# Kernel tuning notes

Hardware: AMD Instinct MI355X
Metric: run time of the kernel (lower is better)

The kernel has to match this reference:

```python
import jax, jax.numpy as jnp
import numpy as np

L = 4


def make_coord(h, w):
    # pixel-center coords in [-1,1], shape (h*w, 2), dim order (y, x)
    ys = -1.0 + 1.0 / h + (2.0 / h) * jnp.arange(h, dtype=jnp.float32)
    xs = -1.0 + 1.0 / w + (2.0 / w) * jnp.arange(w, dtype=jnp.float32)
    gy, gx = jnp.meshgrid(ys, xs, indexing='ij')
    return jnp.stack([gy, gx], axis=-1).reshape(-1, 2)


def bilinear_sample(feat, gx, gy):
    # feat: (B,C,H,W); gx,gy in [-1,1], shape (B,N); align_corners=True
    B, C, H, W = feat.shape
    ix = (gx + 1.0) * 0.5 * (W - 1)
    iy = (gy + 1.0) * 0.5 * (H - 1)
    x0f = jnp.floor(ix)
    y0f = jnp.floor(iy)
    x0 = jnp.clip(x0f.astype(jnp.int32), 0, W - 1)
    x1 = jnp.clip(x0 + 1, 0, W - 1)
    y0 = jnp.clip(y0f.astype(jnp.int32), 0, H - 1)
    y1 = jnp.clip(y0 + 1, 0, H - 1)
    wx1 = ix - x0f
    wx0 = 1.0 - wx1
    wy1 = iy - y0f
    wy0 = 1.0 - wy1
    featf = feat.reshape(B, C, H * W)

    def g(yi, xi):
        idx = yi * W + xi  # (B,N)
        return jnp.take_along_axis(featf, idx[:, None, :], axis=2)  # (B,C,N)

    out = (g(y0, x0) * (wy0 * wx0)[:, None, :] + g(y0, x1) * (wy0 * wx1)[:, None, :]
           + g(y1, x0) * (wy1 * wx0)[:, None, :] + g(y1, x1) * (wy1 * wx1)[:, None, :])
    return out.transpose(0, 2, 1)  # (B,N,C)


def pos_enc(x):
    # x: (B,N,2) -> (B,N,4L); per dim: [sin_0..sin_{L-1}, cos_0..cos_{L-1}]
    freq = (2.0 ** jnp.arange(L, dtype=jnp.float32)) * np.pi
    spec = x[..., None] * freq  # (B,N,2,L)
    enc = jnp.concatenate([jnp.sin(spec), jnp.cos(spec)], axis=-1)  # (B,N,2,2L)
    return enc.reshape(*x.shape[:-1], 4 * L)


def mlp(x, w0, b0, w1, b1, w2, b2, w3, b3):
    h = jax.nn.relu(x @ w0 + b0)
    h = jax.nn.relu(h @ w1 + b1)
    h = jax.nn.relu(h @ w2 + b2)
    return h @ w3 + b3


def setup_inputs() -> dict:
    key = jax.random.key(0)
    ks = jax.random.split(key, 8)
    B, C, H, W = 4, 64, 128, 128
    hid, out_dim = 256, 3
    in_dim = C + 2 + 4 * L + 2  # 84
    s = 0.05
    return {
        'inp': jax.random.normal(ks[0], (B, C, H, W), jnp.float32),
        'w0': jax.random.normal(ks[1], (in_dim, hid), jnp.float32) * s,
        'b0': jnp.zeros((hid,), jnp.float32),
        'w1': jax.random.normal(ks[2], (hid, hid), jnp.float32) * s,
        'b1': jnp.zeros((hid,), jnp.float32),
        'w2': jax.random.normal(ks[3], (hid, hid), jnp.float32) * s,
        'b2': jnp.zeros((hid,), jnp.float32),
        'w3': jax.random.normal(ks[4], (hid, out_dim), jnp.float32) * s,
        'b3': jnp.zeros((out_dim,), jnp.float32),
        'scale': 2,
    }


def reference(inp, w0, b0, w1, b1, w2, b2, w3, b3, scale):
    B, C, H, W = inp.shape
    th, tw = int(round(H * scale)), int(round(W * scale))
    N = th * tw
    coord = jnp.broadcast_to(make_coord(th, tw)[None], (B, N, 2))
    # cell = (2/th, 2/tw); rel_cell = cell * (H, W)
    rel_cell = jnp.broadcast_to(
        jnp.array([2.0 / th * H, 2.0 / tw * W], jnp.float32), (B, N, 2))
    # feature-pixel coordinate map, appended as extra channels so one gather serves both
    fc = make_coord(H, W).reshape(H, W, 2).transpose(2, 0, 1)  # (2,H,W)
    aug = jnp.concatenate([inp, jnp.broadcast_to(fc[None], (B, 2, H, W))], axis=1)

    pe = pos_enc(coord)  # same for all 4 ensemble branches
    hw_scale = jnp.array([H, W], jnp.float32)
    rx, ry = 1.0 / H, 1.0 / W
    eps = 1e-6

    preds, areas = [], []
    for vx in (-1, 1):
        for vy in (-1, 1):
            c0 = jnp.clip(coord[..., 0] + vx * rx + eps, -1 + 1e-6, 1 - 1e-6)
            c1 = jnp.clip(coord[..., 1] + vy * ry + eps, -1 + 1e-6, 1 - 1e-6)
            # grid_sample uses (x, y) = flipped coord -> gx=c1, gy=c0
            q = bilinear_sample(aug, c1, c0)  # (B,N,C+2)
            q_feat, q_coord = q[..., :C], q[..., C:]
            rel = (coord - q_coord) * hw_scale  # (B,N,2)
            x = jnp.concatenate([q_feat, rel, pe, rel_cell], axis=-1)
            preds.append(mlp(x, w0, b0, w1, b1, w2, b2, w3, b3))
            areas.append(jnp.abs(rel[..., 0] * rel[..., 1]) + 1e-9)

    areas = [areas[3], areas[2], areas[1], areas[0]]  # diagonal swap
    tot = areas[0] + areas[1] + areas[2] + areas[3]
    ret = sum(p * (a / tot)[..., None] for p, a in zip(preds, areas))  # (B,N,out)
    return ret.reshape(B, th, tw, -1).transpose(0, 3, 1, 2)  # (B,out,th,tw)
```

## Files before the change

### kernel.cpp

```cpp
#include <hip/hip_runtime.h>
#include <math.h>

#define NB 4
#define NH 128
#define NW 128
#define TH 256
#define TW 256
#define AST 264
#define K0 96
#define MROWS 256
#define PIXB 64

typedef _Float16 f16;
typedef f16  f16x8 __attribute__((ext_vector_type(8)));
typedef f16  f16x4v __attribute__((ext_vector_type(4)));
typedef float f32x4 __attribute__((ext_vector_type(4)));
typedef float f32x16 __attribute__((ext_vector_type(16)));

#define OFF_W1 24576
#define OFF_W2 (OFF_W1 + 65536)
#define OFF_W3 (OFF_W2 + 65536)
#define OFF_PE (OFF_W3 + 4096)
#define WS_W_ELEMS (OFF_PE + 4096)
#define FT_ELEMS (NB * NH * NW * 64)

__device__ __forceinline__ void gload_lds16(const f16* g, f16* l) {
  __builtin_amdgcn_global_load_lds(
      (const __attribute__((address_space(1))) void*)(g),
      (__attribute__((address_space(3))) void*)(l), 16, 0, 0);
}

__global__ void cvt_weights(const float* __restrict__ w0, const float* __restrict__ w1,
                            const float* __restrict__ w2, const float* __restrict__ w3,
                            f16* __restrict__ ws) {
  const int i = blockIdx.x * 256 + threadIdx.x;
  if (i < 24576) {
    const int n = i / 96, k = i - n * 96;
    ws[i] = (k < 84) ? (f16)w0[k * 256 + n] : (f16)0.f;
  } else if (i < OFF_W2) {
    const int j = i - OFF_W1; const int n = j >> 8, k = j & 255;
    ws[i] = (f16)w1[k * 256 + n];
  } else if (i < OFF_W3) {
    const int j = i - OFF_W2; const int n = j >> 8, k = j & 255;
    ws[i] = (f16)w2[k * 256 + n];
  } else if (i < OFF_PE) {
    const int j = i - OFF_W3; const int n = j >> 8, k = j & 255;
    ws[i] = (n < 3) ? (f16)w3[k * 3 + n] : (f16)0.f;
  } else if (i < WS_W_ELEMS) {
    const int j = i - OFF_PE;
    const int o = (j & 2047) >> 3, e = j & 7;
    const float c = (2.0f * o + 1.0f) / 256.0f - 1.0f;
    const float f = (float)(1 << (e & 3)) * (float)M_PI;
    ws[i] = (f16)((e < 4) ? sinf(c * f) : cosf(c * f));
  }
}

__global__ void transpose_feat(const float* __restrict__ feat, f16* __restrict__ ft) {
  __shared__ f16 tile[64][66];
  const int bid = blockIdx.x;
  const int xt = bid & 1, y = (bid >> 1) & 127, b = bid >> 8;
  const int x0 = xt * 64;
  {
    const int c4 = threadIdx.x >> 6, x = threadIdx.x & 63;
#pragma unroll
    for (int co = 0; co < 16; ++co) {
      const int c = co * 4 + c4;
      tile[x][c] = (f16)feat[((size_t)(b * 64 + c) * NH + y) * NW + x0 + x];
    }
  }
  __syncthreads();
  {
    const int x4 = threadIdx.x >> 6, c = threadIdx.x & 63;
#pragma unroll
    for (int xo = 0; xo < 16; ++xo) {
      const int x = xo * 4 + x4;
      ft[((size_t)(b * NH + y) * NW + x0 + x) * 64 + c] = tile[x][c];
    }
  }
}

template<int K>
__device__ __forceinline__ void dense_layer(const f16* __restrict__ Wt,
                                            const float* __restrict__ bias,
                                            f16* act, f16* wlds,
                                            int wm, int wn, int l, int tid) {
  constexpr int NK = K / 16;
  const int lo = l & 31, hi = l >> 5;
  const int sn = tid & 255, sh = tid >> 8;
  const f16* src = Wt + (size_t)sn * K + sh * 8;
  f16* wdst = wlds + (tid >> 6) * 512;
  const f16* Bbase = act + (wm * 128 + lo) * AST + hi * 8;

  f32x16 acc[2][4];
#pragma unroll
  for (int nt = 0; nt < 2; ++nt) {
    f32x16 ci;
#pragma unroll
    for (int g = 0; g < 4; ++g) {
      const float4 b4 = *(const float4*)(bias + wn * 64 + nt * 32 + 8 * g + 4 * hi);
      ci[4 * g + 0] = b4.x; ci[4 * g + 1] = b4.y; ci[4 * g + 2] = b4.z; ci[4 * g + 3] = b4.w;
    }
#pragma unroll
    for (int mt = 0; mt < 4; ++mt) acc[nt][mt] = ci;
  }

  gload_lds16(src + 0 * 16, wdst + 0 * 4096);
  gload_lds16(src + 1 * 16, wdst + 1 * 4096);
  asm volatile("s_waitcnt vmcnt(1)" ::: "memory");
  __builtin_amdgcn_s_barrier();

#pragma unroll
  for (int ks = 0; ks < NK; ++ks) {
    if (ks + 2 < NK)
      gload_lds16(src + (ks + 2) * 16, wdst + ((ks + 2) % 3) * 4096);

    const f16* wb = wlds + (ks % 3) * 4096 + hi * 2048;
    const f16x8 A0 = *(const f16x8*)(wb + (wn * 64 + 0 * 32 + lo) * 8);
    const f16x8 A1 = *(const f16x8*)(wb + (wn * 64 + 1 * 32 + lo) * 8);
    const f16x8 B0 = *(const f16x8*)(Bbase + 0 * 32 * AST + ks * 16);
    const f16x8 B1 = *(const f16x8*)(Bbase + 1 * 32 * AST + ks * 16);
    const f16x8 B2 = *(const f16x8*)(Bbase + 2 * 32 * AST + ks * 16);
    const f16x8 B3 = *(const f16x8*)(Bbase + 3 * 32 * AST + ks * 16);

    __builtin_amdgcn_s_setprio(1);
    acc[0][0] = __builtin_amdgcn_mfma_f32_32x32x16_f16(A0, B0, acc[0][0], 0, 0, 0);
    acc[0][1] = __builtin_amdgcn_mfma_f32_32x32x16_f16(A0, B1, acc[0][1], 0, 0, 0);
    acc[0][2] = __builtin_amdgcn_mfma_f32_32x32x16_f16(A0, B2, acc[0][2], 0, 0, 0);
    acc[0][3] = __builtin_amdgcn_mfma_f32_32x32x16_f16(A0, B3, acc[0][3], 0, 0, 0);
    acc[1][0] = __builtin_amdgcn_mfma_f32_32x32x16_f16(A1, B0, acc[1][0], 0, 0, 0);
    acc[1][1] = __builtin_amdgcn_mfma_f32_32x32x16_f16(A1, B1, acc[1][1], 0, 0, 0);
    acc[1][2] = __builtin_amdgcn_mfma_f32_32x32x16_f16(A1, B2, acc[1][2], 0, 0, 0);
    acc[1][3] = __builtin_amdgcn_mfma_f32_32x32x16_f16(A1, B3, acc[1][3], 0, 0, 0);
    __builtin_amdgcn_s_setprio(0);

    asm volatile("s_waitcnt vmcnt(1)" ::: "memory");
    __builtin_amdgcn_s_barrier();
  }

#pragma unroll
  for (int nt = 0; nt < 2; ++nt)
#pragma unroll
    for (int mt = 0; mt < 4; ++mt)
#pragma unroll
      for (int g = 0; g < 4; ++g) {
        f16x4v o;
        o[0] = (f16)fmaxf(acc[nt][mt][4 * g + 0], 0.f);
        o[1] = (f16)fmaxf(acc[nt][mt][4 * g + 1], 0.f);
        o[2] = (f16)fmaxf(acc[nt][mt][4 * g + 2], 0.f);
        o[3] = (f16)fmaxf(acc[nt][mt][4 * g + 3], 0.f);
        *(f16x4v*)(act + (size_t)(wm * 128 + mt * 32 + lo) * AST +
                   wn * 64 + nt * 32 + 8 * g + 4 * hi) = o;
      }
}

template<bool USE_FT>
__global__ __launch_bounds__(512, 2) void inr2d_mfma(
    const float* __restrict__ feat, const f16* __restrict__ ft,
    const float* __restrict__ b0, const float* __restrict__ b1,
    const float* __restrict__ b2, const float* __restrict__ b3,
    const f16* __restrict__ ws, float* __restrict__ out)
{
  __shared__ f16 act[MROWS][AST];
  __shared__ f16 wlds[3 * 4096];
  __shared__ float area_s[MROWS];
  __shared__ f16 pred_s[MROWS][4];

  const int t = threadIdx.x;
  const int blk = ((blockIdx.x & 7) << 9) | (blockIdx.x >> 3);

  {
    const int r = t >> 1, sub = t & 1;
    const int pix = r >> 2, e = r & 3;
    const int gp = blk * PIXB + pix;
    const int b = gp >> 16, rem = gp & 65535;
    const int oy = rem >> 8, ox = rem & 255;

    const float cy = (2.0f * oy + 1.0f) / (float)TH - 1.0f;
    const float cx = (2.0f * ox + 1.0f) / (float)TW - 1.0f;
    const float vx = (e & 2) ? 1.0f : -1.0f;
    const float vy = (e & 1) ? 1.0f : -1.0f;
    const float rr = 1.0f / (float)NH;

    float c0 = fminf(fmaxf(cy + vx * rr + 1e-6f, -1.0f + 1e-6f), 1.0f - 1e-6f);
    float c1 = fminf(fmaxf(cx + vy * rr + 1e-6f, -1.0f + 1e-6f), 1.0f - 1e-6f);

    const float ix = (c1 + 1.0f) * 0.5f * (float)(NW - 1);
    const float iy = (c0 + 1.0f) * 0.5f * (float)(NH - 1);
    const float x0f = floorf(ix), y0f = floorf(iy);
    int x0 = (int)x0f; x0 = max(0, min(x0, NW - 1));
    int x1 = min(x0 + 1, NW - 1);
    int y0 = (int)y0f; y0 = max(0, min(y0, NH - 1));
    int y1 = min(y0 + 1, NH - 1);
    const float wx1 = ix - x0f, wx0 = 1.0f - wx1;
    const float wy1 = iy - y0f, wy0 = 1.0f - wy1;
    const float w00 = wy0 * wx0, w01 = wy0 * wx1, w10 = wy1 * wx0, w11 = wy1 * wx1;

    if (USE_FT) {
      const f16* fb = ft + (size_t)b * (NH * NW * 64);
      const f16* r00 = fb + (size_t)(y0 * NW + x0) * 64 + sub * 32;
      const f16* r01 = fb + (size_t)(y0 * NW + x1) * 64 + sub * 32;
      const f16* r10 = fb + (size_t)(y1 * NW + x0) * 64 + sub * 32;
      const f16* r11 = fb + (size_t)(y1 * NW + x1) * 64 + sub * 32;
#pragma unroll
      for (int h = 0; h < 4; ++h) {
        const f16x8 a00 = *(const f16x8*)(r00 + h * 8);
        const f16x8 a01 = *(const f16x8*)(r01 + h * 8);
        const f16x8 a10 = *(const f16x8*)(r10 + h * 8);
        const f16x8 a11 = *(const f16x8*)(r11 + h * 8);
#pragma unroll
        for (int i = 0; i < 8; ++i) {
          const float v = w00 * (float)a00[i] + w01 * (float)a01[i] +
                          w10 * (float)a10[i] + w11 * (float)a11[i];
          act[r][sub * 32 + h * 8 + i] = (f16)v;
        }
      }
    } else {
      const float* fb = feat + (size_t)b * 64 * NH * NW;
      const int i00 = y0 * NW + x0, i01 = y0 * NW + x1;
      const int i10 = y1 * NW + x0, i11 = y1 * NW + x1;
#pragma unroll
      for (int i = 0; i < 32; ++i) {
        const int c = sub * 32 + i;
        const float* fc = fb + (size_t)c * (NH * NW);
        const float v = w00 * fc[i00] + w01 * fc[i01] + w10 * fc[i10] + w11 * fc[i11];
        act[r][c] = (f16)v;
      }
    }
    if (sub == 0) {
      const float qy = -1.0f + 1.0f / NH + (2.0f / NH) * (wy0 * (float)y0 + wy1 * (float)y1);
      const float qx = -1.0f + 1.0f / NW + (2.0f / NW) * (wx0 * (float)x0 + wx1 * (float)x1);
      const float rely = (cy - qy) * (float)NH;
      const float relx = (cx - qx) * (float)NW;
      act[r][64] = (f16)rely;
      act[r][65] = (f16)relx;
      if (USE_FT) {
        const f16* py = ws + OFF_PE + (size_t)oy * 8;
        const f16* px = ws + OFF_PE + 2048 + (size_t)ox * 8;
#pragma unroll
        for (int j = 0; j < 8; ++j) { act[r][66 + j] = py[j]; act[r][74 + j] = px[j]; }
      } else {
#pragma unroll
        for (int ll = 0; ll < 4; ++ll) {
          const float f = (float)(1 << ll) * (float)M_PI;
          act[r][66 + ll] = (f16)sinf(cy * f);
          act[r][70 + ll] = (f16)cosf(cy * f);
          act[r][74 + ll] = (f16)sinf(cx * f);
          act[r][78 + ll] = (f16)cosf(cx * f);
        }
      }
      act[r][82] = (f16)1.0f;
      act[r][83] = (f16)1.0f;
#pragma unroll
      for (int z = 84; z < K0; ++z) act[r][z] = (f16)0.f;
      area_s[r] = fabsf(rely * relx) + 1e-9f;
    }
  }
  __syncthreads();

  const int w = t >> 6, l = t & 63;
  const int wm = w >> 2, wn = w & 3;

  dense_layer<K0 >(ws,          b0, &act[0][0], wlds, wm, wn, l, t);
  __syncthreads();
  dense_layer<256>(ws + OFF_W1, b1, &act[0][0], wlds, wm, wn, l, t);
  __syncthreads();
  dense_layer<256>(ws + OFF_W2, b2, &act[0][0], wlds, wm, wn, l, t);
  __syncthreads();

  {
    const int nl = l & 15, kq = l >> 4;
    const f16* Abase = ws + OFF_W3 + nl * 256 + kq * 8;
#pragma unroll
    for (int p = 0; p < 2; ++p) {
      const f16* Bbase2 = &act[w * 32 + p * 16 + nl][0] + kq * 8;
      f32x4 acc = {0.f, 0.f, 0.f, 0.f};
#pragma unroll
      for (int ks = 0; ks < 8; ++ks) {
        f16x8 a = *(const f16x8*)(Abase + ks * 32);
        f16x8 b = *(const f16x8*)(Bbase2 + ks * 32);
        acc = __builtin_amdgcn_mfma_f32_16x16x32_f16(a, b, acc, 0, 0, 0);
      }
      if (l < 16) {
        f16x4v pr;
        pr[0] = (f16)(acc[0] + b3[0]); pr[1] = (f16)(acc[1] + b3[1]);
        pr[2] = (f16)(acc[2] + b3[2]); pr[3] = (f16)0.f;
        *(f16x4v*)(&pred_s[w * 32 + p * 16 + l][0]) = pr;
      }
    }
  }
  __syncthreads();

  if (t < PIXB * 3) {
    const int pix = t / 3, o = t - pix * 3;
    const int gp = blk * PIXB + pix;
    const int b = gp >> 16, rem = gp & 65535;
    const int oy = rem >> 8, ox = rem & 255;
    const int r0 = pix * 4;
    const float a0 = area_s[r0], a1 = area_s[r0 + 1], a2 = area_s[r0 + 2], a3 = area_s[r0 + 3];
    const float tot = a0 + a1 + a2 + a3;
    const float v = (float)pred_s[r0][o] * a3 + (float)pred_s[r0 + 1][o] * a2 +
                    (float)pred_s[r0 + 2][o] * a1 + (float)pred_s[r0 + 3][o] * a0;
    out[(((size_t)b * 3 + o) << 16) + (oy << 8) + ox] = v / tot;
  }
}

extern "C" void kernel_launch(void* const* d_in, const int* in_sizes, int n_in,
                              void* d_out, int out_size, void* d_ws, size_t ws_size,
                              hipStream_t stream) {
  const float* feat = (const float*)d_in[0];
  const float* w0 = (const float*)d_in[1];
  const float* b0 = (const float*)d_in[2];
  const float* w1 = (const float*)d_in[3];
  const float* b1 = (const float*)d_in[4];
  const float* w2 = (const float*)d_in[5];
  const float* b2 = (const float*)d_in[6];
  const float* w3 = (const float*)d_in[7];
  const float* b3 = (const float*)d_in[8];
  float* out = (float*)d_out;
  f16* ws = (f16*)d_ws;

  cvt_weights<<<(WS_W_ELEMS + 255) / 256, 256, 0, stream>>>(w0, w1, w2, w3, ws);

  const int blocks = (NB * TH * TW) / PIXB;
  const bool use_ft = ws_size >= (size_t)(WS_W_ELEMS + FT_ELEMS) * sizeof(f16);
  if (use_ft) {
    f16* ft = ws + WS_W_ELEMS;
    transpose_feat<<<NB * NH * (NW / 64), 256, 0, stream>>>(feat, ft);
    inr2d_mfma<true><<<blocks, 512, 0, stream>>>(feat, ft, b0, b1, b2, b3, ws, out);
  } else {
    inr2d_mfma<false><<<blocks, 512, 0, stream>>>(feat, nullptr, b0, b1, b2, b3, ws, out);
  }
}
```

Measured before the change: 437.5 us.

## Halve block tile, swizzle activation LDS, double-buffer weights, recompute areas

Shrinks each block from 512 threads and 64 pixels to 256 threads and 32 pixels. The activation buffer becomes unpadded with an XOR swizzle instead of row padding, and the weight staging drops from a triple to a double buffer. Each wave's tile changes to a 64x128 output slice (4 A-fragments, 2 B-fragments), and ensemble areas are recomputed in the epilogue instead of stored in LDS, with prediction scratch aliased onto the weight buffer. The aim is a smaller LDS footprint for more resident blocks, plus conflict-free activation reads. The cost is a shallower prefetch pipeline with a full vmcnt(0) wait each step, and more barriers per unit of work.

```diff
diff --git a/kernel.cpp b/kernel.cpp
--- a/kernel.cpp
+++ b/kernel.cpp
@@ -6,10 +6,9 @@
 #define NW 128
 #define TH 256
 #define TW 256
-#define AST 264
 #define K0 96
-#define MROWS 256
-#define PIXB 64
+#define MROWS 128
+#define PIXB 32
 
 typedef _Float16 f16;
 typedef f16  f16x8 __attribute__((ext_vector_type(8)));
@@ -23,6 +22,10 @@
 #define OFF_PE (OFF_W3 + 4096)
 #define WS_W_ELEMS (OFF_PE + 4096)
 #define FT_ELEMS (NB * NH * NW * 64)
+
+__device__ __forceinline__ int act_off(int row, int colByte) {
+  return row * 512 + (colByte ^ ((row & 7) << 4));
+}
 
 __device__ __forceinline__ void gload_lds16(const f16* g, f16* l) {
   __builtin_amdgcn_global_load_lds(
@@ -82,65 +85,73 @@
 template<int K>
 __device__ __forceinline__ void dense_layer(const f16* __restrict__ Wt,
                                             const float* __restrict__ bias,
-                                            f16* act, f16* wlds,
+                                            char* actc, f16* wlds,
                                             int wm, int wn, int l, int tid) {
   constexpr int NK = K / 16;
   const int lo = l & 31, hi = l >> 5;
-  const int sn = tid & 255, sh = tid >> 8;
-  const f16* src = Wt + (size_t)sn * K + sh * 8;
+  const f16* src = Wt + (size_t)tid * K;
   f16* wdst = wlds + (tid >> 6) * 512;
-  const f16* Bbase = act + (wm * 128 + lo) * AST + hi * 8;
-
-  f32x16 acc[2][4];
-#pragma unroll
-  for (int nt = 0; nt < 2; ++nt) {
+
+  f32x16 acc[4][2];
+#pragma unroll
+  for (int nt = 0; nt < 4; ++nt) {
     f32x16 ci;
 #pragma unroll
     for (int g = 0; g < 4; ++g) {
-      const float4 b4 = *(const float4*)(bias + wn * 64 + nt * 32 + 8 * g + 4 * hi);
+      const float4 b4 = *(const float4*)(bias + wn * 128 + nt * 32 + 8 * g + 4 * hi);
       ci[4 * g + 0] = b4.x; ci[4 * g + 1] = b4.y; ci[4 * g + 2] = b4.z; ci[4 * g + 3] = b4.w;
     }
 #pragma unroll
-    for (int mt = 0; mt < 4; ++mt) acc[nt][mt] = ci;
-  }
-
-  gload_lds16(src + 0 * 16, wdst + 0 * 4096);
-  gload_lds16(src + 1 * 16, wdst + 1 * 4096);
-  asm volatile("s_waitcnt vmcnt(1)" ::: "memory");
+    for (int mt = 0; mt < 2; ++mt) acc[nt][mt] = ci;
+  }
+
+  gload_lds16(src + 0 * 16 + 0, wdst);
+  gload_lds16(src + 0 * 16 + 8, wdst + 2048);
+  asm volatile("s_waitcnt vmcnt(0)" ::: "memory");
   __builtin_amdgcn_s_barrier();
+  asm volatile("" ::: "memory");
 
 #pragma unroll
   for (int ks = 0; ks < NK; ++ks) {
-    if (ks + 2 < NK)
-      gload_lds16(src + (ks + 2) * 16, wdst + ((ks + 2) % 3) * 4096);
-
-    const f16* wb = wlds + (ks % 3) * 4096 + hi * 2048;
-    const f16x8 A0 = *(const f16x8*)(wb + (wn * 64 + 0 * 32 + lo) * 8);
-    const f16x8 A1 = *(const f16x8*)(wb + (wn * 64 + 1 * 32 + lo) * 8);
-    const f16x8 B0 = *(const f16x8*)(Bbase + 0 * 32 * AST + ks * 16);
-    const f16x8 B1 = *(const f16x8*)(Bbase + 1 * 32 * AST + ks * 16);
-    const f16x8 B2 = *(const f16x8*)(Bbase + 2 * 32 * AST + ks * 16);
-    const f16x8 B3 = *(const f16x8*)(Bbase + 3 * 32 * AST + ks * 16);
+    const int buf = ks & 1;
+    if (ks + 1 < NK) {
+      f16* d = wdst + ((ks + 1) & 1) * 4096;
+      gload_lds16(src + (ks + 1) * 16 + 0, d);
+      gload_lds16(src + (ks + 1) * 16 + 8, d + 2048);
+    }
+    const f16* wb = wlds + buf * 4096 + hi * 2048 + (wn * 128 + lo) * 8;
+    const f16x8 A0 = *(const f16x8*)(wb + 0 * 32 * 8);
+    const f16x8 A1 = *(const f16x8*)(wb + 1 * 32 * 8);
+    const f16x8 A2 = *(const f16x8*)(wb + 2 * 32 * 8);
+    const f16x8 A3 = *(const f16x8*)(wb + 3 * 32 * 8);
+    const int cb = ks * 32 + hi * 16;
+    const f16x8 B0 = *(const f16x8*)(actc + act_off(wm * 64 + 0 * 32 + lo, cb));
+    const f16x8 B1 = *(const f16x8*)(actc + act_off(wm * 64 + 1 * 32 + lo, cb));
+
+    asm volatile("s_waitcnt lgkmcnt(0)" ::: "memory");
+    __builtin_amdgcn_sched_barrier(0);
 
     __builtin_amdgcn_s_setprio(1);
     acc[0][0] = __builtin_amdgcn_mfma_f32_32x32x16_f16(A0, B0, acc[0][0], 0, 0, 0);
     acc[0][1] = __builtin_amdgcn_mfma_f32_32x32x16_f16(A0, B1, acc[0][1], 0, 0, 0);
-    acc[0][2] = __builtin_amdgcn_mfma_f32_32x32x16_f16(A0, B2, acc[0][2], 0, 0, 0);
-    acc[0][3] = __builtin_amdgcn_mfma_f32_32x32x16_f16(A0, B3, acc[0][3], 0, 0, 0);
     acc[1][0] = __builtin_amdgcn_mfma_f32_32x32x16_f16(A1, B0, acc[1][0], 0, 0, 0);
     acc[1][1] = __builtin_amdgcn_mfma_f32_32x32x16_f16(A1, B1, acc[1][1], 0, 0, 0);
-    acc[1][2] = __builtin_amdgcn_mfma_f32_32x32x16_f16(A1, B2, acc[1][2], 0, 0, 0);
-    acc[1][3] = __builtin_amdgcn_mfma_f32_32x32x16_f16(A1, B3, acc[1][3], 0, 0, 0);
+    acc[2][0] = __builtin_amdgcn_mfma_f32_32x32x16_f16(A2, B0, acc[2][0], 0, 0, 0);
+    acc[2][1] = __builtin_amdgcn_mfma_f32_32x32x16_f16(A2, B1, acc[2][1], 0, 0, 0);
+    acc[3][0] = __builtin_amdgcn_mfma_f32_32x32x16_f16(A3, B0, acc[3][0], 0, 0, 0);
+    acc[3][1] = __builtin_amdgcn_mfma_f32_32x32x16_f16(A3, B1, acc[3][1], 0, 0, 0);
     __builtin_amdgcn_s_setprio(0);
 
-    asm volatile("s_waitcnt vmcnt(1)" ::: "memory");
+    if (ks + 1 < NK)
+      asm volatile("s_waitcnt vmcnt(0)" ::: "memory");
     __builtin_amdgcn_s_barrier();
-  }
-
-#pragma unroll
-  for (int nt = 0; nt < 2; ++nt)
-#pragma unroll
-    for (int mt = 0; mt < 4; ++mt)
+    asm volatile("" ::: "memory");
+  }
+
+#pragma unroll
+  for (int nt = 0; nt < 4; ++nt)
+#pragma unroll
+    for (int mt = 0; mt < 2; ++mt)
 #pragma unroll
       for (int g = 0; g < 4; ++g) {
         f16x4v o;
@@ -148,25 +159,26 @@
         o[1] = (f16)fmaxf(acc[nt][mt][4 * g + 1], 0.f);
         o[2] = (f16)fmaxf(acc[nt][mt][4 * g + 2], 0.f);
         o[3] = (f16)fmaxf(acc[nt][mt][4 * g + 3], 0.f);
-        *(f16x4v*)(act + (size_t)(wm * 128 + mt * 32 + lo) * AST +
-                   wn * 64 + nt * 32 + 8 * g + 4 * hi) = o;
+        const int row = wm * 64 + mt * 32 + lo;
+        const int colB = wn * 256 + nt * 64 + 16 * g + 8 * hi;
+        *(f16x4v*)(actc + act_off(row, colB)) = o;
       }
 }
 
 template<bool USE_FT>
-__global__ __launch_bounds__(512, 2) void inr2d_mfma(
+__global__ __launch_bounds__(256, 2) void inr2d_mfma(
     const float* __restrict__ feat, const f16* __restrict__ ft,
     const float* __restrict__ b0, const float* __restrict__ b1,
     const float* __restrict__ b2, const float* __restrict__ b3,
     const f16* __restrict__ ws, float* __restrict__ out)
 {
-  __shared__ f16 act[MROWS][AST];
-  __shared__ f16 wlds[3 * 4096];
-  __shared__ float area_s[MROWS];
-  __shared__ f16 pred_s[MROWS][4];
-
+  __shared__ f16 act[MROWS * 256];
+  __shared__ f16 wlds[2 * 4096];
+  f16 (*pred_s)[4] = (f16(*)[4])wlds;
+
+  char* actc = (char*)act;
   const int t = threadIdx.x;
-  const int blk = ((blockIdx.x & 7) << 9) | (blockIdx.x >> 3);
+  const int blk = ((blockIdx.x & 7) << 10) | (blockIdx.x >> 3);
 
   {
     const int r = t >> 1, sub = t & 1;
@@ -207,12 +219,13 @@
         const f16x8 a01 = *(const f16x8*)(r01 + h * 8);
         const f16x8 a10 = *(const f16x8*)(r10 + h * 8);
         const f16x8 a11 = *(const f16x8*)(r11 + h * 8);
+        f16x8 o;
 #pragma unroll
         for (int i = 0; i < 8; ++i) {
-          const float v = w00 * (float)a00[i] + w01 * (float)a01[i] +
-                          w10 * (float)a10[i] + w11 * (float)a11[i];
-          act[r][sub * 32 + h * 8 + i] = (f16)v;
+          o[i] = (f16)(w00 * (float)a00[i] + w01 * (float)a01[i] +
+                       w10 * (float)a10[i] + w11 * (float)a11[i]);
         }
+        *(f16x8*)(actc + act_off(r, 64 * sub + 16 * h)) = o;
       }
     } else {
       const float* fb = feat + (size_t)b * 64 * NH * NW;
@@ -223,7 +236,7 @@
         const int c = sub * 32 + i;
         const float* fc = fb + (size_t)c * (NH * NW);
         const float v = w00 * fc[i00] + w01 * fc[i01] + w10 * fc[i10] + w11 * fc[i11];
-        act[r][c] = (f16)v;
+        *(f16*)(actc + act_off(r, 2 * c)) = (f16)v;
       }
     }
     if (sub == 0) {
@@ -231,40 +244,42 @@
       const float qx = -1.0f + 1.0f / NW + (2.0f / NW) * (wx0 * (float)x0 + wx1 * (float)x1);
       const float rely = (cy - qy) * (float)NH;
       const float relx = (cx - qx) * (float)NW;
-      act[r][64] = (f16)rely;
-      act[r][65] = (f16)relx;
+      *(f16*)(actc + act_off(r, 2 * 64)) = (f16)rely;
+      *(f16*)(actc + act_off(r, 2 * 65)) = (f16)relx;
       if (USE_FT) {
         const f16* py = ws + OFF_PE + (size_t)oy * 8;
         const f16* px = ws + OFF_PE + 2048 + (size_t)ox * 8;
 #pragma unroll
-        for (int j = 0; j < 8; ++j) { act[r][66 + j] = py[j]; act[r][74 + j] = px[j]; }
+        for (int j = 0; j < 8; ++j) {
+          *(f16*)(actc + act_off(r, 2 * (66 + j))) = py[j];
+          *(f16*)(actc + act_off(r, 2 * (74 + j))) = px[j];
+        }
       } else {
 #pragma unroll
         for (int ll = 0; ll < 4; ++ll) {
           const float f = (float)(1 << ll) * (float)M_PI;
-          act[r][66 + ll] = (f16)sinf(cy * f);
-          act[r][70 + ll] = (f16)cosf(cy * f);
-          act[r][74 + ll] = (f16)sinf(cx * f);
-          act[r][78 + ll] = (f16)cosf(cx * f);
+          *(f16*)(actc + act_off(r, 2 * (66 + ll))) = (f16)sinf(cy * f);
+          *(f16*)(actc + act_off(r, 2 * (70 + ll))) = (f16)cosf(cy * f);
+          *(f16*)(actc + act_off(r, 2 * (74 + ll))) = (f16)sinf(cx * f);
+          *(f16*)(actc + act_off(r, 2 * (78 + ll))) = (f16)cosf(cx * f);
         }
       }
-      act[r][82] = (f16)1.0f;
-      act[r][83] = (f16)1.0f;
-#pragma unroll
-      for (int z = 84; z < K0; ++z) act[r][z] = (f16)0.f;
-      area_s[r] = fabsf(rely * relx) + 1e-9f;
+      *(f16*)(actc + act_off(r, 2 * 82)) = (f16)1.0f;
+      *(f16*)(actc + act_off(r, 2 * 83)) = (f16)1.0f;
+#pragma unroll
+      for (int z = 84; z < K0; ++z) *(f16*)(actc + act_off(r, 2 * z)) = (f16)0.f;
     }
   }
   __syncthreads();
 
   const int w = t >> 6, l = t & 63;
-  const int wm = w >> 2, wn = w & 3;
-
-  dense_layer<K0 >(ws,          b0, &act[0][0], wlds, wm, wn, l, t);
-  __syncthreads();
-  dense_layer<256>(ws + OFF_W1, b1, &act[0][0], wlds, wm, wn, l, t);
-  __syncthreads();
-  dense_layer<256>(ws + OFF_W2, b2, &act[0][0], wlds, wm, wn, l, t);
+  const int wm = w >> 1, wn = w & 1;
+
+  dense_layer<K0 >(ws,          b0, actc, wlds, wm, wn, l, t);
+  __syncthreads();
+  dense_layer<256>(ws + OFF_W1, b1, actc, wlds, wm, wn, l, t);
+  __syncthreads();
+  dense_layer<256>(ws + OFF_W2, b2, actc, wlds, wm, wn, l, t);
   __syncthreads();
 
   {
@@ -272,12 +287,12 @@
     const f16* Abase = ws + OFF_W3 + nl * 256 + kq * 8;
 #pragma unroll
     for (int p = 0; p < 2; ++p) {
-      const f16* Bbase2 = &act[w * 32 + p * 16 + nl][0] + kq * 8;
+      const int row = w * 32 + p * 16 + nl;
       f32x4 acc = {0.f, 0.f, 0.f, 0.f};
 #pragma unroll
       for (int ks = 0; ks < 8; ++ks) {
         f16x8 a = *(const f16x8*)(Abase + ks * 32);
-        f16x8 b = *(const f16x8*)(Bbase2 + ks * 32);
+        f16x8 b = *(const f16x8*)(actc + act_off(row, 64 * ks + 16 * kq));
         acc = __builtin_amdgcn_mfma_f32_16x16x32_f16(a, b, acc, 0, 0, 0);
       }
       if (l < 16) {
@@ -295,11 +310,35 @@
     const int gp = blk * PIXB + pix;
     const int b = gp >> 16, rem = gp & 65535;
     const int oy = rem >> 8, ox = rem & 255;
+    const float cy = (2.0f * oy + 1.0f) / (float)TH - 1.0f;
+    const float cx = (2.0f * ox + 1.0f) / (float)TW - 1.0f;
+    const float rr = 1.0f / (float)NH;
+    float ar[4];
+#pragma unroll
+    for (int e = 0; e < 4; ++e) {
+      const float vx = (e & 2) ? 1.0f : -1.0f;
+      const float vy = (e & 1) ? 1.0f : -1.0f;
+      float c0 = fminf(fmaxf(cy + vx * rr + 1e-6f, -1.0f + 1e-6f), 1.0f - 1e-6f);
+      float c1 = fminf(fmaxf(cx + vy * rr + 1e-6f, -1.0f + 1e-6f), 1.0f - 1e-6f);
+      const float ix = (c1 + 1.0f) * 0.5f * (float)(NW - 1);
+      const float iy = (c0 + 1.0f) * 0.5f * (float)(NH - 1);
+      const float x0f = floorf(ix), y0f = floorf(iy);
+      int x0 = (int)x0f; x0 = max(0, min(x0, NW - 1));
+      int x1 = min(x0 + 1, NW - 1);
+      int y0 = (int)y0f; y0 = max(0, min(y0, NH - 1));
+      int y1 = min(y0 + 1, NH - 1);
+      const float wx1 = ix - x0f, wx0 = 1.0f - wx1;
+      const float wy1 = iy - y0f, wy0 = 1.0f - wy1;
+      const float qy = -1.0f + 1.0f / NH + (2.0f / NH) * (wy0 * (float)y0 + wy1 * (float)y1);
+      const float qx = -1.0f + 1.0f / NW + (2.0f / NW) * (wx0 * (float)x0 + wx1 * (float)x1);
+      const float rely = (cy - qy) * (float)NH;
+      const float relx = (cx - qx) * (float)NW;
+      ar[e] = fabsf(rely * relx) + 1e-9f;
+    }
     const int r0 = pix * 4;
-    const float a0 = area_s[r0], a1 = area_s[r0 + 1], a2 = area_s[r0 + 2], a3 = area_s[r0 + 3];
-    const float tot = a0 + a1 + a2 + a3;
-    const float v = (float)pred_s[r0][o] * a3 + (float)pred_s[r0 + 1][o] * a2 +
-                    (float)pred_s[r0 + 2][o] * a1 + (float)pred_s[r0 + 3][o] * a0;
+    const float tot = ar[0] + ar[1] + ar[2] + ar[3];
+    const float v = (float)pred_s[r0][o] * ar[3] + (float)pred_s[r0 + 1][o] * ar[2] +
+                    (float)pred_s[r0 + 2][o] * ar[1] + (float)pred_s[r0 + 3][o] * ar[0];
     out[(((size_t)b * 3 + o) << 16) + (oy << 8) + ox] = v / tot;
   }
 }
@@ -326,8 +365,8 @@
   if (use_ft) {
     f16* ft = ws + WS_W_ELEMS;
     transpose_feat<<<NB * NH * (NW / 64), 256, 0, stream>>>(feat, ft);
-    inr2d_mfma<true><<<blocks, 512, 0, stream>>>(feat, ft, b0, b1, b2, b3, ws, out);
+    inr2d_mfma<true><<<blocks, 256, 0, stream>>>(feat, ft, b0, b1, b2, b3, ws, out);
   } else {
-    inr2d_mfma<false><<<blocks, 512, 0, stream>>>(feat, nullptr, b0, b1, b2, b3, ws, out);
-  }
-}
+    inr2d_mfma<false><<<blocks, 256, 0, stream>>>(feat, nullptr, b0, b1, b2, b3, ws, out);
+  }
+}
```

After: 537.0 us. 22.7% more time.
